# Kernel tuning notes

Hardware: AMD Instinct MI355X
Metric: run time of the kernel (lower is better)

## Reference

```python
import jax, jax.numpy as jnp
import numpy as np

NUM_EMBEDDINGS = 1024
EMBEDDING_DIM = 256


def setup_inputs() -> dict:
    key = jax.random.key(0)
    k1, k2 = jax.random.split(key)
    z = jax.random.normal(k1, (32, EMBEDDING_DIM, 32, 32), dtype=jnp.float32)
    codebook = jax.random.normal(k2, (NUM_EMBEDDINGS, EMBEDDING_DIM), dtype=jnp.float32)
    return {"z": z, "codebook": codebook}


def reference(z, codebook):
    # z: (B, C, H, W) -> (B, H, W, C) -> (B*H*W, C)
    B, C, H, W = z.shape
    z_bhwc = jnp.transpose(z, (0, 2, 3, 1))
    z_flat = z_bhwc.reshape(-1, C)  # (N, C)

    # pairwise squared distances: ||z||^2 + ||e||^2 - 2 z.e^T  -> (N, K)
    distances = (
        jnp.sum(z_flat ** 2, axis=1, keepdims=True)
        + jnp.sum(codebook ** 2, axis=1)
        - 2.0 * jnp.matmul(z_flat, codebook.T)
    )
    argmin_codewords = jnp.argmin(distances, axis=1)  # (N,)
    min_codewords = jax.nn.one_hot(argmin_codewords, NUM_EMBEDDINGS, dtype=jnp.float32)  # (N, K)

    # quantized latents via one-hot @ codebook, back to (B, C, H, W)
    z_quantized = jnp.matmul(min_codewords, codebook).reshape(B, H, W, C)
    z_quantized = jnp.transpose(z_quantized, (0, 3, 1, 2))
    return (min_codewords, z_quantized)
```

## Files before the change

### kernel.cpp

```cpp
#include <hip/hip_runtime.h>

#define N_ROWS 32768
#define K_CODES 1024
#define CDIM 256

typedef _Float16 half8 __attribute__((ext_vector_type(8)));
typedef _Float16 half4 __attribute__((ext_vector_type(4)));
typedef float floatx16 __attribute__((ext_vector_type(16)));
typedef unsigned long long ull;

#define WS_ZH   0ull
#define WS_ZL   16777216ull
#define WS_CBH  33554432ull
#define WS_CBL  34078720ull
#define WS_CBN  34603008ull
#define WS_PART 34607104ull
#define WS_IDX  36704256ull
#define WS_NEED 36835328ull

__device__ __forceinline__ void g2lds16(const void* g, void* l) {
    __builtin_amdgcn_global_load_lds(
        (const __attribute__((address_space(1))) void*)g,
        (__attribute__((address_space(3))) void*)l, 16, 0, 0);
}

__global__ __launch_bounds__(256) void prep_all(const float* __restrict__ z,
                                                const float* __restrict__ cb,
                                                _Float16* __restrict__ zh,
                                                _Float16* __restrict__ zl,
                                                _Float16* __restrict__ cbh,
                                                _Float16* __restrict__ cbl,
                                                float* __restrict__ cbn,
                                                ull* __restrict__ part) {
    __shared__ float t[64][68];
    if (blockIdx.x >= 2048) {
        int k = ((blockIdx.x - 2048) << 2) | (threadIdx.x >> 6);
        int lane = threadIdx.x & 63;
        float4 v = reinterpret_cast<const float4*>(cb + k * CDIM)[lane];
        float s0 = v.x * 32.f, s1 = v.y * 32.f, s2 = v.z * 32.f, s3 = v.w * 32.f;
        half4 hv, lv;
        hv[0] = (_Float16)s0; lv[0] = (_Float16)(s0 - (float)hv[0]);
        hv[1] = (_Float16)s1; lv[1] = (_Float16)(s1 - (float)hv[1]);
        hv[2] = (_Float16)s2; lv[2] = (_Float16)(s2 - (float)hv[2]);
        hv[3] = (_Float16)s3; lv[3] = (_Float16)(s3 - (float)hv[3]);
        size_t off = (size_t)((lane >> 1) * K_CODES + k) * 8 + ((lane & 1) * 4);
        *reinterpret_cast<half4*>(&cbh[off]) = hv;
        *reinterpret_cast<half4*>(&cbl[off]) = lv;
        float s = s0 * s0 + s1 * s1 + s2 * s2 + s3 * s3;
        #pragma unroll
        for (int off2 = 32; off2 > 0; off2 >>= 1) s += __shfl_down(s, off2);
        if (lane == 0) cbn[k] = s;
        return;
    }
    if (threadIdx.x < 16) part[blockIdx.x * 16 + threadIdx.x] = ~0ull;

    int hwt = blockIdx.x & 15;
    int ct  = (blockIdx.x >> 4) & 3;
    int bb  = blockIdx.x >> 6;
    int tid = threadIdx.x;
    #pragma unroll
    for (int p = 0; p < 4; p++) {
        int e = p * 256 + tid;
        int c = e >> 4, h4 = e & 15;
        float4 v = *reinterpret_cast<const float4*>(
            &z[((bb * 256 + ct * 64 + c) << 10) + hwt * 64 + h4 * 4]);
        *reinterpret_cast<float4*>(&t[c][h4 * 4]) = v;
    }
    __syncthreads();
    #pragma unroll
    for (int p = 0; p < 4; p++) {
        int e = p * 256 + tid;
        int hw = e >> 4, c4 = e & 15;
        half4 hv, lv;
        #pragma unroll
        for (int j = 0; j < 4; j++) {
            float s = t[c4 * 4 + j][hw] * 32.f;
            _Float16 h = (_Float16)s;
            hv[j] = h;
            lv[j] = (_Float16)(s - (float)h);
        }
        int n = bb * 1024 + hwt * 64 + hw;
        int cg = ct * 64 + c4 * 4;
        size_t off = (size_t)((cg >> 3) * N_ROWS + n) * 8 + (cg & 7);
        *reinterpret_cast<half4*>(&zh[off]) = hv;
        *reinterpret_cast<half4*>(&zl[off]) = lv;
    }
}

__global__ __launch_bounds__(256, 4) void vq_db(
    const _Float16* __restrict__ zh, const _Float16* __restrict__ zl,
    const _Float16* __restrict__ cbh, const _Float16* __restrict__ cbl,
    const float* __restrict__ cbn, ull* __restrict__ part) {

    __shared__ _Float16 AhL[2][2048], AlL[2][2048];
    __shared__ _Float16 BhL[2][2048], BlL[2][2048];

    const int tid = threadIdx.x;
    const int lane = tid & 63, wave = tid >> 6;
    const int wm = wave & 1, wn = wave >> 1;
    const int fm = lane & 31, fq = lane >> 5;
    const int L = (blockIdx.x & 7) * 256 + (blockIdx.x >> 3);
    const int codeTile = L & 7;
    const int rowTile  = L >> 3;
    const int rowBase = rowTile * 128, codeBase = codeTile * 128;

    floatx16 acc[4];
    #pragma unroll
    for (int i = 0; i < 4; i++) acc[i] = (floatx16)0.f;

    const int p_ = tid >> 7, r_ = tid & 127;
    auto stage = [&](int buf, int ch) {
        const size_t ao = ((size_t)(ch * 2 + p_) * N_ROWS + rowBase + r_) * 8;
        const size_t bo = ((size_t)(ch * 2 + p_) * K_CODES + codeBase + r_) * 8;
        g2lds16(zh + ao,  &AhL[buf][tid * 8]);
        g2lds16(zl + ao,  &AlL[buf][tid * 8]);
        g2lds16(cbh + bo, &BhL[buf][tid * 8]);
        g2lds16(cbl + bo, &BlL[buf][tid * 8]);
    };
    auto compute = [&](int buf) {
        half8 ah[2], al[2], bh[2], bl[2];
        #pragma unroll
        for (int i = 0; i < 2; i++) {
            int ga = fq * 128 + wm * 64 + i * 32 + fm;
            ah[i] = *reinterpret_cast<const half8*>(&AhL[buf][ga * 8]);
            al[i] = *reinterpret_cast<const half8*>(&AlL[buf][ga * 8]);
        }
        #pragma unroll
        for (int j = 0; j < 2; j++) {
            int gb = fq * 128 + wn * 64 + j * 32 + fm;
            bh[j] = *reinterpret_cast<const half8*>(&BhL[buf][gb * 8]);
            bl[j] = *reinterpret_cast<const half8*>(&BlL[buf][gb * 8]);
        }
        #pragma unroll
        for (int i = 0; i < 2; i++)
            #pragma unroll
            for (int j = 0; j < 2; j++) {
                acc[i*2+j] = __builtin_amdgcn_mfma_f32_32x32x16_f16(ah[i], bh[j], acc[i*2+j], 0, 0, 0);
                acc[i*2+j] = __builtin_amdgcn_mfma_f32_32x32x16_f16(al[i], bh[j], acc[i*2+j], 0, 0, 0);
                acc[i*2+j] = __builtin_amdgcn_mfma_f32_32x32x16_f16(ah[i], bl[j], acc[i*2+j], 0, 0, 0);
            }
    };

    stage(0, 0);
    __syncthreads();
    for (int c = 0; c < 16; c += 2) {
        stage(1, c + 1);
        compute(0);
        __syncthreads();
        if (c + 2 < 16) stage(0, c + 2);
        compute(1);
        __syncthreads();
    }

    float cbnv[2];
    #pragma unroll
    for (int j = 0; j < 2; j++) cbnv[j] = cbn[codeBase + wn * 64 + j * 32 + fm];

    #pragma unroll
    for (int i = 0; i < 2; i++)
        #pragma unroll
        for (int r = 0; r < 16; r++) {
            float best = 3.4e38f; int bcode = 0x7fffffff;
            #pragma unroll
            for (int j = 0; j < 2; j++) {
                float d = fmaf(-2.f, acc[i*2+j][r], cbnv[j]);
                int code = codeBase + wn * 64 + j * 32 + fm;
                if (d < best) { best = d; bcode = code; }
            }
            #pragma unroll
            for (int m = 1; m < 32; m <<= 1) {
                float ov = __shfl_xor(best, m, 64);
                int   oc = __shfl_xor(bcode, m, 64);
                if (ov < best || (ov == best && oc < bcode)) { best = ov; bcode = oc; }
            }
            if (fm == 0) {
                int row = rowBase + wm * 64 + i * 32 + (r & 3) + 8 * (r >> 2) + 4 * fq;
                unsigned u = __float_as_uint(best);
                u = (u & 0x80000000u) ? ~u : (u | 0x80000000u);
                atomicMin(&part[row], ((ull)u << 32) | (unsigned)bcode);
            }
        }
}

__global__ __launch_bounds__(256) void onehot_fin3(const ull* __restrict__ part,
                                                   int* __restrict__ idx,
                                                   float* __restrict__ out) {
    __shared__ int sid[16];
    const int rb = blockIdx.x * 16;
    const int tid = threadIdx.x;
    if (tid < 16) {
        int id = (int)(part[rb + tid] & 0xffffffffu);
        sid[tid] = id;
        idx[rb + tid] = id;
    }
    __syncthreads();
    const int k4 = tid << 2;
    #pragma unroll
    for (int r = 0; r < 16; r++) {
        int id = sid[r];
        float4 v4;
        v4.x = (k4     == id) ? 1.f : 0.f;
        v4.y = (k4 + 1 == id) ? 1.f : 0.f;
        v4.z = (k4 + 2 == id) ? 1.f : 0.f;
        v4.w = (k4 + 3 == id) ? 1.f : 0.f;
        reinterpret_cast<float4*>(out)[(size_t)(rb + r) * 256 + tid] = v4;
    }
}

__global__ __launch_bounds__(256) void zq_fill2(const int* __restrict__ idx,
                                                const float* __restrict__ cb,
                                                float* __restrict__ out) {
    __shared__ float tile[64][257];
    const int tid = threadIdx.x;
    const int n0 = (blockIdx.x >> 2) << 8;
    const int c0 = (blockIdx.x & 3) << 6;
    const int b  = n0 >> 10;
    const int hw0 = n0 & 1023;

    const int id = idx[n0 + tid];
    const float4* cb4 = reinterpret_cast<const float4*>(cb);
    #pragma unroll
    for (int jj = 0; jj < 16; jj++) {
        float4 v = cb4[id * 64 + (c0 >> 2) + jj];
        tile[jj * 4 + 0][tid] = v.x;
        tile[jj * 4 + 1][tid] = v.y;
        tile[jj * 4 + 2][tid] = v.z;
        tile[jj * 4 + 3][tid] = v.w;
    }
    __syncthreads();
    #pragma unroll
    for (int c = 0; c < 64; c++) {
        out[((size_t)(b * 256 + c0 + c) << 10) + hw0 + tid] = tile[c][tid];
    }
}


__global__ __launch_bounds__(64) void cb_norms(const float* __restrict__ cb,
                                               float* __restrict__ cbn) {
    int k = blockIdx.x;
    int lane = threadIdx.x;
    float4 v = reinterpret_cast<const float4*>(cb + k * CDIM)[lane];
    float s = v.x * v.x + v.y * v.y + v.z * v.z + v.w * v.w;
    #pragma unroll
    for (int off = 32; off > 0; off >>= 1) s += __shfl_down(s, off);
    if (lane == 0) cbn[k] = s;
}

__global__ __launch_bounds__(256) void cb_transpose(const float* __restrict__ cb,
                                                    float* __restrict__ cbt) {
    __shared__ float t[32][33];
    int k0 = (blockIdx.x & 31) * 32;
    int c0 = (blockIdx.x >> 5) * 32;
    int lane = threadIdx.x & 31;
    int row = threadIdx.x >> 5;
    #pragma unroll
    for (int s = 0; s < 4; s++) {
        int r = row + s * 8;
        t[r][lane] = cb[(k0 + r) * CDIM + c0 + lane];
    }
    __syncthreads();
    #pragma unroll
    for (int s = 0; s < 4; s++) {
        int r = row + s * 8;
        cbt[(c0 + r) * K_CODES + k0 + lane] = t[lane][r];
    }
}

__global__ __launch_bounds__(512, 2) void vq_argmin(const float* __restrict__ z,
                                                    const float* __restrict__ cbt,
                                                    const float* __restrict__ cbn,
                                                    int* __restrict__ idx_out) {
    __shared__ float As[64][128];
    __shared__ float Bs[64][256];

    const int tid = threadIdx.x;
    const int tx = tid & 31;
    const int ty = tid >> 5;
    const int rowBase = blockIdx.x * 128;
    const int bb = rowBase >> 10;
    const int hwBase = rowBase & 1023;

    float minv[8];
    int   mini[8];
    #pragma unroll
    for (int i = 0; i < 8; i++) { minv[i] = 3.4e38f; mini[i] = 0; }

    for (int kt = 0; kt < K_CODES; kt += 256) {
        float acc[2][2][4][4];
        #pragma unroll
        for (int a = 0; a < 2; a++)
            #pragma unroll
            for (int b = 0; b < 2; b++)
                #pragma unroll
                for (int i = 0; i < 4; i++)
                    #pragma unroll
                    for (int j = 0; j < 4; j++) acc[a][b][i][j] = 0.f;

        for (int ccb = 0; ccb < CDIM; ccb += 64) {
            #pragma unroll
            for (int l = 0; l < 4; l++) {
                int f = tid + l * 512;
                int r4 = f & 31, c = f >> 5;
                float4 v = *reinterpret_cast<const float4*>(
                    &z[((bb * 256 + ccb + c) << 10) + hwBase + r4 * 4]);
                *reinterpret_cast<float4*>(&As[c][r4 * 4]) = v;
            }
            #pragma unroll
            for (int l = 0; l < 8; l++) {
                int f = tid + l * 512;
                int k4 = f & 63, c = f >> 6;
                float4 v = *reinterpret_cast<const float4*>(
                    &cbt[(ccb + c) * K_CODES + kt + k4 * 4]);
                *reinterpret_cast<float4*>(&Bs[c][k4 * 4]) = v;
            }
            __syncthreads();
            #pragma unroll 4
            for (int c = 0; c < 64; c++) {
                float4 a0 = *reinterpret_cast<const float4*>(&As[c][ty * 4]);
                float4 a1 = *reinterpret_cast<const float4*>(&As[c][64 + ty * 4]);
                float4 b0 = *reinterpret_cast<const float4*>(&Bs[c][tx * 4]);
                float4 b1 = *reinterpret_cast<const float4*>(&Bs[c][128 + tx * 4]);
                float av[2][4] = {{a0.x, a0.y, a0.z, a0.w}, {a1.x, a1.y, a1.z, a1.w}};
                float bw[2][4] = {{b0.x, b0.y, b0.z, b0.w}, {b1.x, b1.y, b1.z, b1.w}};
                #pragma unroll
                for (int ri = 0; ri < 2; ri++)
                    #pragma unroll
                    for (int i = 0; i < 4; i++)
                        #pragma unroll
                        for (int ci = 0; ci < 2; ci++)
                            #pragma unroll
                            for (int j = 0; j < 4; j++)
                                acc[ri][ci][i][j] =
                                    fmaf(av[ri][i], bw[ci][j], acc[ri][ci][i][j]);
            }
            __syncthreads();
        }
        #pragma unroll
        for (int ci = 0; ci < 2; ci++)
            #pragma unroll
            for (int j = 0; j < 4; j++) {
                int code = kt + ci * 128 + tx * 4 + j;
                float nrm = cbn[code];
                #pragma unroll
                for (int ri = 0; ri < 2; ri++)
                    #pragma unroll
                    for (int i = 0; i < 4; i++) {
                        float d = fmaf(-2.f, acc[ri][ci][i][j], nrm);
                        int r = ri * 4 + i;
                        if (d < minv[r]) { minv[r] = d; mini[r] = code; }
                    }
            }
    }

    __syncthreads();
    float (*rv)[32] = reinterpret_cast<float(*)[32]>(&As[0][0]);
    int   (*rix)[32] = reinterpret_cast<int(*)[32]>(&As[32][0]);
    #pragma unroll
    for (int ri = 0; ri < 2; ri++)
        #pragma unroll
        for (int i = 0; i < 4; i++) {
            int row = ri * 64 + ty * 4 + i;
            rv[row][tx] = minv[ri * 4 + i];
            rix[row][tx] = mini[ri * 4 + i];
        }
    __syncthreads();
    if (tid < 128) {
        float bvv = rv[tid][0]; int bii = rix[tid][0];
        #pragma unroll
        for (int t = 1; t < 32; t++) {
            float v = rv[tid][t]; int ii = rix[tid][t];
            if (v < bvv || (v == bvv && ii < bii)) { bvv = v; bii = ii; }
        }
        idx_out[rowBase + tid] = bii;
    }
}

__global__ __launch_bounds__(256) void onehot_fill(const int* __restrict__ idx,
                                                   float* __restrict__ out) {
    int i = blockIdx.x * 256 + threadIdx.x;
    int n  = i >> 8;
    int k4 = (i & 255) << 2;
    int id = idx[n];
    float4 v;
    v.x = (k4     == id) ? 1.f : 0.f;
    v.y = (k4 + 1 == id) ? 1.f : 0.f;
    v.z = (k4 + 2 == id) ? 1.f : 0.f;
    v.w = (k4 + 3 == id) ? 1.f : 0.f;
    reinterpret_cast<float4*>(out)[i] = v;
}

extern "C" void kernel_launch(void* const* d_in, const int* in_sizes, int n_in,
                              void* d_out, int out_size, void* d_ws, size_t ws_size,
                              hipStream_t stream) {
    const float* z  = (const float*)d_in[0];
    const float* cb = (const float*)d_in[1];
    float* out0 = (float*)d_out;
    float* out1 = out0 + (size_t)N_ROWS * K_CODES;

    if (ws_size >= WS_NEED) {
        _Float16* zh  = (_Float16*)((char*)d_ws + WS_ZH);
        _Float16* zl  = (_Float16*)((char*)d_ws + WS_ZL);
        _Float16* cbh = (_Float16*)((char*)d_ws + WS_CBH);
        _Float16* cbl = (_Float16*)((char*)d_ws + WS_CBL);
        float* cbn = (float*)((char*)d_ws + WS_CBN);
        ull* part = (ull*)((char*)d_ws + WS_PART);
        int* idx = (int*)((char*)d_ws + WS_IDX);

        prep_all<<<2304, 256, 0, stream>>>(z, cb, zh, zl, cbh, cbl, cbn, part);
        vq_db<<<2048, 256, 0, stream>>>(zh, zl, cbh, cbl, cbn, part);
        onehot_fin3<<<2048, 256, 0, stream>>>(part, idx, out0);
        zq_fill2<<<512, 256, 0, stream>>>(idx, cb, out1);
    } else {
        float* cbn = (float*)d_ws;
        int*   idx = (int*)((char*)d_ws + 4096);
        float* cbt = (float*)((char*)d_ws + 4096 + 131072);

        cb_norms<<<K_CODES, 64, 0, stream>>>(cb, cbn);
        cb_transpose<<<256, 256, 0, stream>>>(cb, cbt);
        vq_argmin<<<N_ROWS / 128, 512, 0, stream>>>(z, cbt, cbn, idx);
        onehot_fill<<<(N_ROWS * K_CODES / 4) / 256, 256, 0, stream>>>(idx, out0);
        zq_fill2<<<512, 256, 0, stream>>>(idx, cb, out1);
    }
}
```

Before: 288.8 us.

## Use explicit vmcnt waits for LDS pipelining and merge finalize kernels

In the fp16 split MFMA kernel, each __syncthreads is replaced by a partial s_waitcnt vmcnt(4) plus a raw s_barrier, fenced by sched_barriers. The next stage's global-to-LDS loads can then stay in flight while the current buffer is consumed, instead of draining every outstanding load. Separately, the one-hot writer and the quantized-latent gather are merged into one finalize launch that reads indices straight from the packed argmin buffer. This removes one launch and the intermediate idx array. The manual waitcnt counts rely on each stage issuing exactly four loads per thread.

```diff
diff --git a/kernel.cpp b/kernel.cpp
--- a/kernel.cpp
+++ b/kernel.cpp
@@ -116,6 +116,7 @@
         g2lds16(zl + ao,  &AlL[buf][tid * 8]);
         g2lds16(cbh + bo, &BhL[buf][tid * 8]);
         g2lds16(cbl + bo, &BlL[buf][tid * 8]);
+        __builtin_amdgcn_sched_barrier(0);
     };
     auto compute = [&](int buf) {
         half8 ah[2], al[2], bh[2], bl[2];
@@ -142,14 +143,27 @@
     };
 
     stage(0, 0);
-    __syncthreads();
     for (int c = 0; c < 16; c += 2) {
         stage(1, c + 1);
+        asm volatile("s_waitcnt vmcnt(4)" ::: "memory");
+        __builtin_amdgcn_sched_barrier(0);
+        __builtin_amdgcn_s_barrier();
+        __builtin_amdgcn_sched_barrier(0);
         compute(0);
-        __syncthreads();
-        if (c + 2 < 16) stage(0, c + 2);
+        __builtin_amdgcn_s_barrier();
+        __builtin_amdgcn_sched_barrier(0);
+        if (c + 2 < 16) {
+            stage(0, c + 2);
+            asm volatile("s_waitcnt vmcnt(4)" ::: "memory");
+        } else {
+            asm volatile("s_waitcnt vmcnt(0)" ::: "memory");
+        }
+        __builtin_amdgcn_sched_barrier(0);
+        __builtin_amdgcn_s_barrier();
+        __builtin_amdgcn_sched_barrier(0);
         compute(1);
-        __syncthreads();
+        __builtin_amdgcn_s_barrier();
+        __builtin_amdgcn_sched_barrier(0);
     }
 
     float cbnv[2];
@@ -182,42 +196,37 @@
         }
 }
 
-__global__ __launch_bounds__(256) void onehot_fin3(const ull* __restrict__ part,
-                                                   int* __restrict__ idx,
-                                                   float* __restrict__ out) {
-    __shared__ int sid[16];
-    const int rb = blockIdx.x * 16;
+__global__ __launch_bounds__(256) void finalize(const ull* __restrict__ part,
+                                                const float* __restrict__ cb,
+                                                float* __restrict__ out0,
+                                                float* __restrict__ out1) {
     const int tid = threadIdx.x;
-    if (tid < 16) {
-        int id = (int)(part[rb + tid] & 0xffffffffu);
-        sid[tid] = id;
-        idx[rb + tid] = id;
-    }
-    __syncthreads();
-    const int k4 = tid << 2;
-    #pragma unroll
-    for (int r = 0; r < 16; r++) {
-        int id = sid[r];
-        float4 v4;
-        v4.x = (k4     == id) ? 1.f : 0.f;
-        v4.y = (k4 + 1 == id) ? 1.f : 0.f;
-        v4.z = (k4 + 2 == id) ? 1.f : 0.f;
-        v4.w = (k4 + 3 == id) ? 1.f : 0.f;
-        reinterpret_cast<float4*>(out)[(size_t)(rb + r) * 256 + tid] = v4;
-    }
-}
-
-__global__ __launch_bounds__(256) void zq_fill2(const int* __restrict__ idx,
-                                                const float* __restrict__ cb,
-                                                float* __restrict__ out) {
+    if (blockIdx.x < 2048) {
+        __shared__ int sid[16];
+        const int rb = blockIdx.x * 16;
+        if (tid < 16) sid[tid] = (int)(part[rb + tid] & 0xffffffffu);
+        __syncthreads();
+        const int k4 = tid << 2;
+        #pragma unroll
+        for (int r = 0; r < 16; r++) {
+            int id = sid[r];
+            float4 v4;
+            v4.x = (k4     == id) ? 1.f : 0.f;
+            v4.y = (k4 + 1 == id) ? 1.f : 0.f;
+            v4.z = (k4 + 2 == id) ? 1.f : 0.f;
+            v4.w = (k4 + 3 == id) ? 1.f : 0.f;
+            reinterpret_cast<float4*>(out0)[(size_t)(rb + r) * 256 + tid] = v4;
+        }
+        return;
+    }
     __shared__ float tile[64][257];
-    const int tid = threadIdx.x;
-    const int n0 = (blockIdx.x >> 2) << 8;
-    const int c0 = (blockIdx.x & 3) << 6;
+    const int blk = blockIdx.x - 2048;
+    const int n0 = (blk >> 2) << 8;
+    const int c0 = (blk & 3) << 6;
     const int b  = n0 >> 10;
     const int hw0 = n0 & 1023;
 
-    const int id = idx[n0 + tid];
+    const int id = (int)(part[n0 + tid] & 0xffffffffu);
     const float4* cb4 = reinterpret_cast<const float4*>(cb);
     #pragma unroll
     for (int jj = 0; jj < 16; jj++) {
@@ -230,7 +239,7 @@
     __syncthreads();
     #pragma unroll
     for (int c = 0; c < 64; c++) {
-        out[((size_t)(b * 256 + c0 + c) << 10) + hw0 + tid] = tile[c][tid];
+        out1[((size_t)(b * 256 + c0 + c) << 10) + hw0 + tid] = tile[c][tid];
     }
 }
 
@@ -389,6 +398,33 @@
     reinterpret_cast<float4*>(out)[i] = v;
 }
 
+__global__ __launch_bounds__(256) void zq_fill2(const int* __restrict__ idx,
+                                                const float* __restrict__ cb,
+                                                float* __restrict__ out) {
+    __shared__ float tile[64][257];
+    const int tid = threadIdx.x;
+    const int n0 = (blockIdx.x >> 2) << 8;
+    const int c0 = (blockIdx.x & 3) << 6;
+    const int b  = n0 >> 10;
+    const int hw0 = n0 & 1023;
+
+    const int id = idx[n0 + tid];
+    const float4* cb4 = reinterpret_cast<const float4*>(cb);
+    #pragma unroll
+    for (int jj = 0; jj < 16; jj++) {
+        float4 v = cb4[id * 64 + (c0 >> 2) + jj];
+        tile[jj * 4 + 0][tid] = v.x;
+        tile[jj * 4 + 1][tid] = v.y;
+        tile[jj * 4 + 2][tid] = v.z;
+        tile[jj * 4 + 3][tid] = v.w;
+    }
+    __syncthreads();
+    #pragma unroll
+    for (int c = 0; c < 64; c++) {
+        out[((size_t)(b * 256 + c0 + c) << 10) + hw0 + tid] = tile[c][tid];
+    }
+}
+
 extern "C" void kernel_launch(void* const* d_in, const int* in_sizes, int n_in,
                               void* d_out, int out_size, void* d_ws, size_t ws_size,
                               hipStream_t stream) {
@@ -404,12 +440,10 @@
         _Float16* cbl = (_Float16*)((char*)d_ws + WS_CBL);
         float* cbn = (float*)((char*)d_ws + WS_CBN);
         ull* part = (ull*)((char*)d_ws + WS_PART);
-        int* idx = (int*)((char*)d_ws + WS_IDX);
 
         prep_all<<<2304, 256, 0, stream>>>(z, cb, zh, zl, cbh, cbl, cbn, part);
         vq_db<<<2048, 256, 0, stream>>>(zh, zl, cbh, cbl, cbn, part);
-        onehot_fin3<<<2048, 256, 0, stream>>>(part, idx, out0);
-        zq_fill2<<<512, 256, 0, stream>>>(idx, cb, out1);
+        finalize<<<2560, 256, 0, stream>>>(part, cb, out0, out1);
     } else {
         float* cbn = (float*)d_ws;
         int*   idx = (int*)((char*)d_ws + 4096);
```

New measurement: 284.1 us. No clear change (-1.6%).
